# Kernel tuning notes

Hardware: AMD Instinct MI355X
Metric: run time of the kernel (lower is better)

Reference implementation:

```python
import jax, jax.numpy as jnp
import numpy as np

N_NODES = 50000
N_EDGES = 800000
IN_C, HID_C, OUT_C = 128, 256, 64


def _linear_params(key, fan_in, fan_out):
    kw, kb = jax.random.split(key)
    bound = 1.0 / np.sqrt(fan_in)
    w = jax.random.uniform(kw, (fan_in, fan_out), jnp.float32, -bound, bound)
    b = jax.random.uniform(kb, (fan_out,), jnp.float32, -bound, bound)
    return w, b


def setup_inputs() -> dict:
    key = jax.random.key(0)
    ks = jax.random.split(key, 8)
    x = jax.random.normal(ks[0], (N_NODES, IN_C), jnp.float32)
    edge_index = jax.random.randint(ks[1], (2, N_EDGES), 0, N_NODES, dtype=jnp.int64)
    w1a, b1a = _linear_params(ks[2], IN_C, HID_C)
    w1b, b1b = _linear_params(ks[3], HID_C, HID_C)
    w2a, b2a = _linear_params(ks[4], HID_C, HID_C)
    w2b, b2b = _linear_params(ks[5], HID_C, HID_C)
    w3a, b3a = _linear_params(ks[6], HID_C, HID_C)
    w3b, b3b = _linear_params(ks[7], HID_C, OUT_C)
    return {
        "x": x, "edge_index": edge_index,
        "w1a": w1a, "b1a": b1a, "w1b": w1b, "b1b": b1b,
        "w2a": w2a, "b2a": b2a, "w2b": w2b, "b2b": b2b,
        "w3a": w3a, "b3a": b3a, "w3b": w3b, "b3b": b3b,
    }


def _gin_conv(x, src, dst, wa, ba, wb, bb):
    # GINConv (eps=0): MLP( x + sum_{j->i} x_j )
    agg = jax.ops.segment_sum(x[src], dst, num_segments=N_NODES)  # [N, d]
    h = x + agg
    h = jnp.maximum(h @ wa + ba, 0.0)
    return h @ wb + bb


def reference(x, edge_index, w1a, b1a, w1b, b1b, w2a, b2a, w2b, b2b,
              w3a, b3a, w3b, b3b):
    src, dst = edge_index[0], edge_index[1]
    h = jnp.maximum(_gin_conv(x, src, dst, w1a, b1a, w1b, b1b), 0.0)
    h = jnp.maximum(_gin_conv(h, src, dst, w2a, b2a, w2b, b2b), 0.0)
    # output head: Linear -> ReLU -> Dropout(eval: identity) -> Linear
    h = jnp.maximum(h @ w3a + b3a, 0.0)
    return h @ w3b + b3b  # [N, OUT_C]
```

## Files before the change

### kernel.cpp

```cpp
#include <hip/hip_runtime.h>
#include <stdint.h>

#define N_NODES 50000
#define N_EDGES 800000
#define M_PAD   50048
#define NREP    4
#define MCAP    8
#define SCAP    24
#define BCAP    (MCAP + SCAP)
#define CSTR    50048
#define NPX     6256

typedef __attribute__((ext_vector_type(8))) short bf16x8;
typedef __attribute__((ext_vector_type(4))) float f32x4;
typedef __attribute__((ext_vector_type(4))) unsigned int u32x4;

__device__ __forceinline__ unsigned short f2b(float f){
    unsigned int u = __builtin_bit_cast(unsigned int, f);
    u += 0x7fffu + ((u >> 16) & 1u);
    return (unsigned short)(u >> 16);
}
__device__ __forceinline__ float b2f(unsigned short s){
    unsigned int u = ((unsigned int)s) << 16;
    return __builtin_bit_cast(float, u);
}
__device__ __forceinline__ float bcf(unsigned int u){
    return __builtin_bit_cast(float, u);
}

__device__ __forceinline__ void gl_lds16(const void* g, void* l){
    __builtin_amdgcn_global_load_lds(
        (const __attribute__((address_space(1))) void*)g,
        (__attribute__((address_space(3))) void*)l, 16, 0, 0);
}

__device__ __forceinline__ int t_off(int row, int us){
    return row * 256 + (((us >> 3) ^ (row & 7)) << 3) + (us & 7);
}

__device__ __forceinline__ void stage_w(const char* __restrict__ Wb, int kt, int K,
                                        int bytes, int tid, char* dst){
    for (int o = tid * 16; o < bytes; o += 8192){
        const int row = o >> 6, gs = ((o & 63) >> 4) ^ (row & 3);
        gl_lds16(Wb + ((size_t)row * K + kt * 32) * 2 + gs * 16, dst + o);
    }
}

__device__ __forceinline__ int pdeg(const int* __restrict__ cnt, int n){
    int v = 0;
#pragma unroll
    for (int r = 0; r < 4; ++r){
        int c = cnt[r * CSTR + n];
        v += (c > BCAP) ? BCAP : c;
    }
    return (v + 3) & ~3;
}

__global__ void k_x2b(const float* __restrict__ x, unsigned short* __restrict__ xs,
                      int* __restrict__ cnt){
    int gi = blockIdx.x * 256 + threadIdx.x;
    if (gi < NREP * CSTR) cnt[gi] = 0;
    size_t e0 = (size_t)gi * 8;
    if (e0 >= (size_t)M_PAD * 128) return;
    int node = (int)(e0 >> 7);
    int ch0  = (int)(e0 & 127);
    int sl = ch0 >> 5, wth = ch0 & 31;
    bf16x8 o;
    if (node < N_NODES){
        const float4* xp = (const float4*)(x + e0);
        float4 a = xp[0], b = xp[1];
        o[0] = (short)f2b(a.x); o[1] = (short)f2b(a.y);
        o[2] = (short)f2b(a.z); o[3] = (short)f2b(a.w);
        o[4] = (short)f2b(b.x); o[5] = (short)f2b(b.y);
        o[6] = (short)f2b(b.z); o[7] = (short)f2b(b.w);
    } else {
#pragma unroll
        for (int i = 0; i < 8; ++i) o[i] = 0;
    }
    *(bf16x8*)&xs[((size_t)(sl * 50048 + node)) * 32 + wth] = o;
}

__global__ __launch_bounds__(256) void k_scatter(const int* __restrict__ ei,
        int* __restrict__ cnt, unsigned short* __restrict__ mn,
        unsigned short* __restrict__ sp){
    const int x = blockIdx.x & 7;
    const int c = blockIdx.x >> 3;
    const int nlo = x * NPX, nhi = nlo + NPX;
    const int r = threadIdx.x & 3;
#pragma unroll
    for (int i = 0; i < 4; ++i){
        int e = c * 1024 + i * 256 + threadIdx.x;
        if (e < N_EDGES){
            int d = ei[N_EDGES + e];
            if (d >= nlo && d < nhi && (unsigned)d < N_NODES){
                unsigned s = (unsigned)ei[e];
                if (s < N_NODES){
                    int p = atomicAdd(&cnt[r * CSTR + d], 1);
                    int b = (d << 2) + r;
                    if (p < MCAP) mn[(b << 3) + p] = (unsigned short)s;
                    else if (p < BCAP) sp[b * SCAP + (p - MCAP)] = (unsigned short)s;
                }
            }
        }
    }
}

__global__ void k_scan1(const int* __restrict__ cnt, int* __restrict__ bsum){
    __shared__ int s[256];
    int t = threadIdx.x, n = blockIdx.x * 256 + t;
    int v = (n < M_PAD) ? pdeg(cnt, n) : 0;
    s[t] = v;
    __syncthreads();
    for (int off = 128; off > 0; off >>= 1){
        if (t < off) s[t] += s[t + off];
        __syncthreads();
    }
    if (t == 0) bsum[blockIdx.x] = s[0];
}

__global__ void k_scan2(const int* __restrict__ bsum, int* __restrict__ boff){
    __shared__ int s[256];
    int t = threadIdx.x;
    int v = (t < 196) ? bsum[t] : 0;
    s[t] = v;
    __syncthreads();
    for (int off = 1; off < 256; off <<= 1){
        int a = (t >= off) ? s[t - off] : 0;
        __syncthreads();
        s[t] += a;
        __syncthreads();
    }
    boff[t] = s[t] - v;
}

__global__ void k_scan3(const int* __restrict__ cnt, const int* __restrict__ boff,
                        int* __restrict__ mgoff){
    __shared__ int s[256];
    int t = threadIdx.x, n = blockIdx.x * 256 + t;
    int v = (n < M_PAD) ? pdeg(cnt, n) : 0;
    s[t] = v;
    __syncthreads();
    for (int off = 1; off < 256; off <<= 1){
        int a = (t >= off) ? s[t - off] : 0;
        __syncthreads();
        s[t] += a;
        __syncthreads();
    }
    if (n < M_PAD) mgoff[n] = boff[blockIdx.x] + s[t] - v;
}

__global__ void k_merge(const int* __restrict__ cnt, const int* __restrict__ mgoff,
                        const unsigned short* __restrict__ mn, const unsigned short* __restrict__ sp,
                        unsigned short* __restrict__ mg, int* __restrict__ mginfo,
                        unsigned short* __restrict__ lperm){
    __shared__ unsigned int keys[64];
    const int t = threadIdx.x;
    const int r = t & 3;
    const int n = blockIdx.x * 64 + (t >> 2);
    int c = cnt[r * CSTR + n];
    if (c > BCAP) c = BCAP;

    const unsigned short* src  = &mn[((n << 2) + r) << 3];
    const unsigned short* ssrc = &sp[((n << 2) + r) * SCAP];
    unsigned short v[BCAP];
    {
        ushort4 m0 = *(const ushort4*)(src);
        ushort4 m1 = *(const ushort4*)(src + 4);
        v[0]=m0.x; v[1]=m0.y; v[2]=m0.z; v[3]=m0.w;
        v[4]=m1.x; v[5]=m1.y; v[6]=m1.z; v[7]=m1.w;
#pragma unroll
        for (int q = 0; q < 6; ++q){
            ushort4 sq = *(const ushort4*)(ssrc + q * 4);
            v[8 + q*4 + 0] = sq.x; v[8 + q*4 + 1] = sq.y;
            v[8 + q*4 + 2] = sq.z; v[8 + q*4 + 3] = sq.w;
        }
    }
#pragma unroll
    for (int i = 0; i < BCAP; ++i)
        if (i >= c) v[i] = 0xFFFFu;

#pragma unroll
    for (int k = 2; k <= 32; k <<= 1){
#pragma unroll
        for (int j = k >> 1; j > 0; j >>= 1){
#pragma unroll
            for (int i = 0; i < 32; ++i){
                const int l = i ^ j;
                if (l > i){
                    const bool up = ((i & k) == 0);
                    unsigned short a = v[i], b = v[l];
                    bool sw = up ? (a > b) : (a < b);
                    unsigned short lo = sw ? b : a, hi = sw ? a : b;
                    v[i] = lo; v[l] = hi;
                }
            }
        }
    }

    int incl = c;
    int t1 = __shfl_up(incl, 1, 4); if (r >= 1) incl += t1;
    int t2 = __shfl_up(incl, 2, 4); if (r >= 2) incl += t2;
    const int excl = incl - c;
    const int total = __shfl(incl, 3, 4);
    const unsigned mb = (unsigned)mgoff[n];
#pragma unroll
    for (int i = 0; i < BCAP; ++i)
        if (i < c) mg[mb + excl + i] = v[i];
    if (r == 3){
        int grp = (total + 3) >> 2;
        mginfo[n] = ((int)mb << 6) | grp;
        for (int pos = total; pos < grp * 4; ++pos) mg[mb + pos] = (unsigned short)N_NODES;
        keys[t >> 2] = ((unsigned)grp << 6) | (unsigned)(t >> 2);
    }
    __syncthreads();
    for (int k = 2; k <= 64; k <<= 1){
        for (int j = k >> 1; j > 0; j >>= 1){
            if (t < 64){
                int l = t ^ j;
                if (l > t){
                    bool up = ((t & k) == 0);
                    unsigned a = keys[t], b = keys[l];
                    if (up ? (a > b) : (a < b)){ keys[t] = b; keys[l] = a; }
                }
            }
            __syncthreads();
        }
    }
    if (t < 64)
        lperm[blockIdx.x * 64 + t] = (unsigned short)(blockIdx.x * 64 + (keys[t] & 63));
}

template<int C, bool SPLIT>
__global__ __launch_bounds__(256) void k_aggx(const unsigned short* __restrict__ in,
        const int* __restrict__ mginfo, const unsigned short* __restrict__ mg,
        const unsigned short* __restrict__ lperm, unsigned short* __restrict__ out){
    constexpr int RS = C / 8;
    const int bid = blockIdx.x, w8 = bid & 7;
    int g, nbase;
    if (SPLIT){ g = w8 & 3; nbase = ((bid >> 3) + (w8 >> 2) * 391) * 64; }
    else      { g = w8;     nbase = (bid >> 3) * 64; }
    const int lane = threadIdx.x & 63, wid = threadIdx.x >> 6;
    const int qd = lane >> 2, lq = lane & 3;
    const int n = (int)lperm[nbase + wid * 16 + qd];
    const u32x4* __restrict__ xr = (const u32x4*)in;
    const unsigned sbu = (unsigned)g * 50048u;

    float alo[4], ahi[4];
    {
        u32x4 s = xr[(sbu + (unsigned)n) * 4u + (unsigned)lq];
#pragma unroll
        for (int j = 0; j < 4; ++j){
            alo[j] = bcf(s[j] << 16);
            ahi[j] = bcf(s[j] & 0xFFFF0000u);
        }
    }
    const int info = mginfo[n];
    const int grp = info & 63;
    const unsigned mbase = (unsigned)(info >> 6);
    for (int k = 0; k < grp; ++k){
        ushort4 jj = *(const ushort4*)&mg[mbase + (unsigned)(k * 4)];
        u32x4 v0 = xr[(sbu + jj.x) * 4u + lq];
        u32x4 v1 = xr[(sbu + jj.y) * 4u + lq];
        u32x4 v2 = xr[(sbu + jj.z) * 4u + lq];
        u32x4 v3 = xr[(sbu + jj.w) * 4u + lq];
#pragma unroll
        for (int j = 0; j < 4; ++j){
            alo[j] += (bcf(v0[j] << 16) + bcf(v1[j] << 16))
                    + (bcf(v2[j] << 16) + bcf(v3[j] << 16));
            ahi[j] += (bcf(v0[j] & 0xFFFF0000u) + bcf(v1[j] & 0xFFFF0000u))
                    + (bcf(v2[j] & 0xFFFF0000u) + bcf(v3[j] & 0xFFFF0000u));
        }
    }
    bf16x8 o;
#pragma unroll
    for (int j = 0; j < 4; ++j){
        o[2*j]     = (short)f2b(alo[j]);
        o[2*j + 1] = (short)f2b(ahi[j]);
    }
    *(bf16x8*)&out[((unsigned)n * RS + (unsigned)(g * 4 + lq)) * 8u] = o;
}

__global__ void k_wt_all(const float* w0, const float* w1, const float* w2,
                         const float* w3, const float* w4, const float* w5,
                         unsigned short* o0, unsigned short* o1, unsigned short* o2,
                         unsigned short* o3, unsigned short* o4, unsigned short* o5){
    const int Ks[6]  = {128, 256, 256, 256, 256, 256};
    const int Ns[6]  = {256, 256, 256, 256, 256,  64};
    const int NPs[6] = {256, 256, 256, 256, 256, 128};
    int s = blockIdx.y;
    const float* w = (s == 0) ? w0 : (s == 1) ? w1 : (s == 2) ? w2
                   : (s == 3) ? w3 : (s == 4) ? w4 : w5;
    unsigned short* o = (s == 0) ? o0 : (s == 1) ? o1 : (s == 2) ? o2
                      : (s == 3) ? o3 : (s == 4) ? o4 : o5;
    int K = Ks[s], N = Ns[s], NP = NPs[s];
    int idx = blockIdx.x * 256 + threadIdx.x;
    if (idx >= NP * K) return;
    int np = idx / K, k = idx - np * K;
    float v = (np < N) ? w[(size_t)k * N + np] : 0.f;
    o[idx] = f2b(v);
}

template<int K1, int NMID, int NOUT, bool RELU_OUT, bool SLICED>
__global__ __launch_bounds__(512) void k_mlp2(const unsigned short* __restrict__ A,
        const unsigned short* __restrict__ WA, const float* __restrict__ bA,
        const unsigned short* __restrict__ WB, const float* __restrict__ bB,
        void* __restrict__ out, int mstore){
    constexpr int NFA = NMID / 64;
    constexpr int NFB = NOUT / 64;
    constexpr int KTA = K1 / 32;
    constexpr int KTB = NMID / 32;
    __shared__ alignas(16) unsigned short As[2][128 * 32];
    __shared__ alignas(16) unsigned short Bs[2][256 * 32];
    __shared__ alignas(16) unsigned short T[128 * 256];
    const int tid  = threadIdx.x;
    const int lane = tid & 63;
    const int wave = tid >> 6;
    const int wm = wave >> 2, wn = wave & 3;
    const int c = lane & 15, qq = lane >> 4;
    const int sc = (qq ^ (c & 3)) * 8;
    const int row0 = blockIdx.x * 128;

    const f32x4 fzero = {0.f, 0.f, 0.f, 0.f};
    const char* Ab = (const char*)A;
    int cur = 0;

    {
        const int o = tid * 16;
        const int row = o >> 6, gs = ((o & 63) >> 4) ^ (row & 3);
        gl_lds16(Ab + ((size_t)(row0 + row) * K1) * 2 + gs * 16, (char*)As[0] + o);
    }
    stage_w((const char*)WA, 0, K1, NMID * 64, tid, (char*)Bs[0]);
    __syncthreads();

    {
        f32x4 acc[NFA][4];
#pragma unroll
        for (int nf = 0; nf < NFA; ++nf)
#pragma unroll
            for (int mf = 0; mf < 4; ++mf) acc[nf][mf] = fzero;
        for (int kt = 0; kt < KTA; ++kt){
            if (kt < KTA - 1){
                const int o = tid * 16;
                const int row = o >> 6, gs = ((o & 63) >> 4) ^ (row & 3);
                gl_lds16(Ab + ((size_t)(row0 + row) * K1 + (kt + 1) * 32) * 2 + gs * 16,
                         (char*)As[cur ^ 1] + o);
                stage_w((const char*)WA, kt + 1, K1, NMID * 64, tid, (char*)Bs[cur ^ 1]);
            } else {
                stage_w((const char*)WB, 0, NMID, NOUT * 64, tid, (char*)Bs[cur ^ 1]);
            }
            const unsigned short* AsC = As[cur];
            const unsigned short* BsC = Bs[cur];
            bf16x8 xf[4];
#pragma unroll
            for (int mf = 0; mf < 4; ++mf)
                xf[mf] = *(const bf16x8*)&AsC[(wm * 64 + mf * 16 + c) * 32 + sc];
#pragma unroll
            for (int nf = 0; nf < NFA; ++nf){
                bf16x8 wf = *(const bf16x8*)&BsC[((wn * NFA + nf) * 16 + c) * 32 + sc];
#pragma unroll
                for (int mf = 0; mf < 4; ++mf)
                    acc[nf][mf] = __builtin_amdgcn_mfma_f32_16x16x32_bf16(wf, xf[mf], acc[nf][mf], 0, 0, 0);
            }
            __syncthreads();
            cur ^= 1;
        }
#pragma unroll
        for (int nf = 0; nf < NFA; ++nf){
            const int nb = wn * (NFA * 16) + nf * 16 + qq * 4;
            const float4 bb = *(const float4*)&bA[nb];
#pragma unroll
            for (int mf = 0; mf < 4; ++mf){
                const int ml = wm * 64 + mf * 16 + c;
                float v0 = fmaxf(acc[nf][mf][0] + bb.x, 0.f);
                float v1 = fmaxf(acc[nf][mf][1] + bb.y, 0.f);
                float v2 = fmaxf(acc[nf][mf][2] + bb.z, 0.f);
                float v3 = fmaxf(acc[nf][mf][3] + bb.w, 0.f);
                uint2 p;
                p.x = (unsigned)f2b(v0) | ((unsigned)f2b(v1) << 16);
                p.y = (unsigned)f2b(v2) | ((unsigned)f2b(v3) << 16);
                *(uint2*)&T[t_off(ml, nb)] = p;
            }
        }
    }
    __syncthreads();

    {
        f32x4 acc[NFB][4];
#pragma unroll
        for (int nf = 0; nf < NFB; ++nf)
#pragma unroll
            for (int mf = 0; mf < 4; ++mf) acc[nf][mf] = fzero;
        for (int kt = 0; kt < KTB; ++kt){
            if (kt < KTB - 1)
                stage_w((const char*)WB, kt + 1, NMID, NOUT * 64, tid, (char*)Bs[cur ^ 1]);
            const unsigned short* BsC = Bs[cur];
            bf16x8 xf[4];
#pragma unroll
            for (int mf = 0; mf < 4; ++mf){
                const int rr = wm * 64 + mf * 16 + c;
                xf[mf] = *(const bf16x8*)&T[t_off(rr, kt * 32 + qq * 8)];
            }
#pragma unroll
            for (int nf = 0; nf < NFB; ++nf){
                bf16x8 wf = *(const bf16x8*)&BsC[((wn * NFB + nf) * 16 + c) * 32 + sc];
#pragma unroll
                for (int mf = 0; mf < 4; ++mf)
                    acc[nf][mf] = __builtin_amdgcn_mfma_f32_16x16x32_bf16(wf, xf[mf], acc[nf][mf], 0, 0, 0);
            }
            __syncthreads();
            cur ^= 1;
        }
#pragma unroll
        for (int nf = 0; nf < NFB; ++nf){
            const int nb = wn * (NFB * 16) + nf * 16 + qq * 4;
            const float4 bb = *(const float4*)&bB[nb];
#pragma unroll
            for (int mf = 0; mf < 4; ++mf){
                const int m = row0 + wm * 64 + mf * 16 + c;
                if (m < mstore){
                    float v0 = acc[nf][mf][0] + bb.x;
                    float v1 = acc[nf][mf][1] + bb.y;
                    float v2 = acc[nf][mf][2] + bb.z;
                    float v3 = acc[nf][mf][3] + bb.w;
                    if (RELU_OUT){
                        v0 = fmaxf(v0, 0.f); v1 = fmaxf(v1, 0.f);
                        v2 = fmaxf(v2, 0.f); v3 = fmaxf(v3, 0.f);
                    }
                    uint2 p;
                    p.x = (unsigned)f2b(v0) | ((unsigned)f2b(v1) << 16);
                    p.y = (unsigned)f2b(v2) | ((unsigned)f2b(v3) << 16);
                    if (SLICED){
                        if (m >= N_NODES){ p.x = 0; p.y = 0; }
                        *(uint2*)&((unsigned short*)out)[
                            ((size_t)((nb >> 5) * 50048 + m)) * 32 + (nb & 31)] = p;
                    } else {
                        *(uint2*)&((unsigned short*)out)[(size_t)m * NOUT + nb] = p;
                    }
                }
            }
        }
    }
}

__global__ __launch_bounds__(512) void k_mlp4(const unsigned short* __restrict__ A,
        const unsigned short* __restrict__ W1, const float* __restrict__ B1,
        const unsigned short* __restrict__ W2, const float* __restrict__ B2,
        const unsigned short* __restrict__ W3, const float* __restrict__ B3,
        const unsigned short* __restrict__ W4, const float* __restrict__ B4,
        float* __restrict__ out){
    __shared__ alignas(16) unsigned short As[2][128 * 32];
    __shared__ alignas(16) unsigned short Bs[2][256 * 32];
    __shared__ alignas(16) unsigned short T[128 * 256];
    const int tid  = threadIdx.x;
    const int lane = tid & 63;
    const int wave = tid >> 6;
    const int wm = wave >> 2, wn = wave & 3;
    const int c = lane & 15, qq = lane >> 4;
    const int sc = (qq ^ (c & 3)) * 8;
    const int row0 = blockIdx.x * 128;
    const f32x4 fzero = {0.f, 0.f, 0.f, 0.f};
    const char* Ab = (const char*)A;
    int cur = 0;

    {
        const int o = tid * 16;
        const int row = o >> 6, gs = ((o & 63) >> 4) ^ (row & 3);
        gl_lds16(Ab + ((size_t)(row0 + row) * 256) * 2 + gs * 16, (char*)As[0] + o);
    }
    stage_w((const char*)W1, 0, 256, 16384, tid, (char*)Bs[0]);
    __syncthreads();

    {
        f32x4 acc[4][4];
#pragma unroll
        for (int nf = 0; nf < 4; ++nf)
#pragma unroll
            for (int mf = 0; mf < 4; ++mf) acc[nf][mf] = fzero;
        for (int kt = 0; kt < 8; ++kt){
            if (kt < 7){
                const int o = tid * 16;
                const int row = o >> 6, gs = ((o & 63) >> 4) ^ (row & 3);
                gl_lds16(Ab + ((size_t)(row0 + row) * 256 + (kt + 1) * 32) * 2 + gs * 16,
                         (char*)As[cur ^ 1] + o);
                stage_w((const char*)W1, kt + 1, 256, 16384, tid, (char*)Bs[cur ^ 1]);
            } else {
                stage_w((const char*)W2, 0, 256, 16384, tid, (char*)Bs[cur ^ 1]);
            }
            const unsigned short* AsC = As[cur];
            const unsigned short* BsC = Bs[cur];
            bf16x8 xf[4];
#pragma unroll
            for (int mf = 0; mf < 4; ++mf)
                xf[mf] = *(const bf16x8*)&AsC[(wm * 64 + mf * 16 + c) * 32 + sc];
#pragma unroll
            for (int nf = 0; nf < 4; ++nf){
                bf16x8 wf = *(const bf16x8*)&BsC[((wn * 4 + nf) * 16 + c) * 32 + sc];
#pragma unroll
                for (int mf = 0; mf < 4; ++mf)
                    acc[nf][mf] = __builtin_amdgcn_mfma_f32_16x16x32_bf16(wf, xf[mf], acc[nf][mf], 0, 0, 0);
            }
            __syncthreads();
            cur ^= 1;
        }
#pragma unroll
        for (int nf = 0; nf < 4; ++nf){
            const int nb = wn * 64 + nf * 16 + qq * 4;
            const float4 bb = *(const float4*)&B1[nb];
#pragma unroll
            for (int mf = 0; mf < 4; ++mf){
                const int ml = wm * 64 + mf * 16 + c;
                float v0 = fmaxf(acc[nf][mf][0] + bb.x, 0.f);
                float v1 = fmaxf(acc[nf][mf][1] + bb.y, 0.f);
                float v2 = fmaxf(acc[nf][mf][2] + bb.z, 0.f);
                float v3 = fmaxf(acc[nf][mf][3] + bb.w, 0.f);
                uint2 p;
                p.x = (unsigned)f2b(v0) | ((unsigned)f2b(v1) << 16);
                p.y = (unsigned)f2b(v2) | ((unsigned)f2b(v3) << 16);
                *(uint2*)&T[t_off(ml, nb)] = p;
            }
        }
    }
    __syncthreads();

#pragma unroll 1
    for (int st = 0; st < 2; ++st){
        const char* Wb    = (const char*)(st == 0 ? W2 : W3);
        const char* Wnext = (const char*)(st == 0 ? W3 : W4);
        const int bytesNext = (st == 0) ? 16384 : 4096;
        const float* Bb = (st == 0 ? B2 : B3);
        f32x4 acc[4][4];
#pragma unroll
        for (int nf = 0; nf < 4; ++nf)
#pragma unroll
            for (int mf = 0; mf < 4; ++mf) acc[nf][mf] = fzero;
        for (int kt = 0; kt < 8; ++kt){
            if (kt < 7) stage_w(Wb, kt + 1, 256, 16384, tid, (char*)Bs[cur ^ 1]);
            else        stage_w(Wnext, 0, 256, bytesNext, tid, (char*)Bs[cur ^ 1]);
            const unsigned short* BsC = Bs[cur];
            bf16x8 xf[4];
#pragma unroll
            for (int mf = 0; mf < 4; ++mf){
                const int rr = wm * 64 + mf * 16 + c;
                xf[mf] = *(const bf16x8*)&T[t_off(rr, kt * 32 + qq * 8)];
            }
#pragma unroll
            for (int nf = 0; nf < 4; ++nf){
                bf16x8 wf = *(const bf16x8*)&BsC[((wn * 4 + nf) * 16 + c) * 32 + sc];
#pragma unroll
                for (int mf = 0; mf < 4; ++mf)
                    acc[nf][mf] = __builtin_amdgcn_mfma_f32_16x16x32_bf16(wf, xf[mf], acc[nf][mf], 0, 0, 0);
            }
            __syncthreads();
            cur ^= 1;
        }
#pragma unroll
        for (int nf = 0; nf < 4; ++nf){
            const int nb = wn * 64 + nf * 16 + qq * 4;
            const float4 bb = *(const float4*)&Bb[nb];
#pragma unroll
            for (int mf = 0; mf < 4; ++mf){
                const int ml = wm * 64 + mf * 16 + c;
                float v0 = fmaxf(acc[nf][mf][0] + bb.x, 0.f);
                float v1 = fmaxf(acc[nf][mf][1] + bb.y, 0.f);
                float v2 = fmaxf(acc[nf][mf][2] + bb.z, 0.f);
                float v3 = fmaxf(acc[nf][mf][3] + bb.w, 0.f);
                uint2 p;
                p.x = (unsigned)f2b(v0) | ((unsigned)f2b(v1) << 16);
                p.y = (unsigned)f2b(v2) | ((unsigned)f2b(v3) << 16);
                *(uint2*)&T[t_off(ml, nb)] = p;
            }
        }
        __syncthreads();
    }

    {
        f32x4 acc[4];
#pragma unroll
        for (int mf = 0; mf < 4; ++mf) acc[mf] = fzero;
        for (int kt = 0; kt < 8; ++kt){
            if (kt < 7) stage_w((const char*)W4, kt + 1, 256, 4096, tid, (char*)Bs[cur ^ 1]);
            const unsigned short* BsC = Bs[cur];
            bf16x8 xf[4];
#pragma unroll
            for (int mf = 0; mf < 4; ++mf){
                const int rr = wm * 64 + mf * 16 + c;
                xf[mf] = *(const bf16x8*)&T[t_off(rr, kt * 32 + qq * 8)];
            }
            bf16x8 wf = *(const bf16x8*)&BsC[(wn * 16 + c) * 32 + sc];
#pragma unroll
            for (int mf = 0; mf < 4; ++mf)
                acc[mf] = __builtin_amdgcn_mfma_f32_16x16x32_bf16(wf, xf[mf], acc[mf], 0, 0, 0);
            __syncthreads();
            cur ^= 1;
        }
        const int nb = wn * 16 + qq * 4;
        const float4 bb = *(const float4*)&B4[nb];
#pragma unroll
        for (int mf = 0; mf < 4; ++mf){
            const int m = row0 + wm * 64 + mf * 16 + c;
            if (m < N_NODES){
                float4 p = make_float4(acc[mf][0] + bb.x, acc[mf][1] + bb.y,
                                       acc[mf][2] + bb.z, acc[mf][3] + bb.w);
                *(float4*)&out[(size_t)m * 64 + nb] = p;
            }
        }
    }
}

extern "C" void kernel_launch(void* const* d_in, const int* in_sizes, int n_in,
                              void* d_out, int out_size, void* d_ws, size_t ws_size,
                              hipStream_t stream){
    const float* x   = (const float*)d_in[0];
    const int*   ei  = (const int*)d_in[1];
    const float* w1a = (const float*)d_in[2];
    const float* b1a = (const float*)d_in[3];
    const float* w1b = (const float*)d_in[4];
    const float* b1b = (const float*)d_in[5];
    const float* w2a = (const float*)d_in[6];
    const float* b2a = (const float*)d_in[7];
    const float* w2b = (const float*)d_in[8];
    const float* b2b = (const float*)d_in[9];
    const float* w3a = (const float*)d_in[10];
    const float* b3a = (const float*)d_in[11];
    const float* w3b = (const float*)d_in[12];
    const float* b3b = (const float*)d_in[13];

    char* ws = (char*)d_ws;
    size_t off = 0;
    auto take = [&](size_t bytes) -> char* {
        off = (off + 255) & ~(size_t)255;
        char* p = ws + off;
        off += bytes;
        return p;
    };
    unsigned short* xs1  = (unsigned short*)take((size_t)4 * 50048 * 32 * 2);
    unsigned short* g1   = (unsigned short*)take((size_t)M_PAD * 128 * 2);
    unsigned short* h1s  = (unsigned short*)take((size_t)8 * 50048 * 32 * 2);
    unsigned short* g2   = (unsigned short*)take((size_t)M_PAD * 256 * 2);
    unsigned short* wt1a = (unsigned short*)take(256 * 128 * 2);
    unsigned short* wt1b = (unsigned short*)take(256 * 256 * 2);
    unsigned short* wt2a = (unsigned short*)take(256 * 256 * 2);
    unsigned short* wt2b = (unsigned short*)take(256 * 256 * 2);
    unsigned short* wt3a = (unsigned short*)take(256 * 256 * 2);
    unsigned short* wt3b = (unsigned short*)take(128 * 256 * 2);
    int*            cnt  = (int*)take((size_t)NREP * CSTR * 4);
    unsigned short* mn   = (unsigned short*)take((size_t)M_PAD * 4 * MCAP * 2);
    unsigned short* sp   = (unsigned short*)take((size_t)M_PAD * 4 * SCAP * 2);
    unsigned short* mg   = (unsigned short*)take((size_t)1100000 * 2);
    int*            mgoff  = (int*)take((size_t)M_PAD * 4);
    int*            mginfo = (int*)take((size_t)M_PAD * 4);
    int*            bsum = (int*)take(256 * 4);
    int*            boff = (int*)take(256 * 4);
    unsigned short* lperm = (unsigned short*)take((size_t)M_PAD * 2);

    k_x2b<<<(M_PAD * 128 / 8 + 255) / 256, 256, 0, stream>>>(x, xs1, cnt);
    k_scatter<<<782 * 8, 256, 0, stream>>>(ei, cnt, mn, sp);
    k_scan1<<<196, 256, 0, stream>>>(cnt, bsum);
    k_scan2<<<1,   256, 0, stream>>>(bsum, boff);
    k_scan3<<<196, 256, 0, stream>>>(cnt, boff, mgoff);
    k_merge<<<782, 256, 0, stream>>>(cnt, mgoff, mn, sp, mg, mginfo, lperm);
    k_wt_all<<<dim3(256, 6), 256, 0, stream>>>(w1a, w1b, w2a, w2b, w3a, w3b,
                                               wt1a, wt1b, wt2a, wt2b, wt3a, wt3b);

    k_aggx<128, true ><<<391 * 8, 256, 0, stream>>>(xs1, mginfo, mg, lperm, g1);
    k_mlp2<128, 256, 256, true, true><<<391, 512, 0, stream>>>(
        g1, wt1a, b1a, wt1b, b1b, h1s, M_PAD);
    k_aggx<256, false><<<782 * 8, 256, 0, stream>>>(h1s, mginfo, mg, lperm, g2);
    k_mlp4<<<391, 512, 0, stream>>>(
        g2, wt2a, b2a, wt2b, b2b, wt3a, b3a, wt3b, b3b, (float*)d_out);
}
```

Measured before the change: 212.2 us.

## Load MLP operands directly from global memory instead of LDS staging

Removes the double-buffered LDS staging of activation and weight tiles in the fused MLP kernels. Each wave now reads its A and W fragments straight from global memory into registers, with the k-loop fully unrolled. This drops the per-k-tile __syncthreads and cuts LDS use from about 112KB to 64KB per block, which may allow more blocks per CU. In exchange, every wave issues redundant global loads of the weights and activations, relying on the L1/L2 caches, and the loads are no longer overlapped with compute through prefetching.

```diff
diff --git a/kernel.cpp b/kernel.cpp
--- a/kernel.cpp
+++ b/kernel.cpp
@@ -36,14 +36,6 @@
 
 __device__ __forceinline__ int t_off(int row, int us){
     return row * 256 + (((us >> 3) ^ (row & 7)) << 3) + (us & 7);
-}
-
-__device__ __forceinline__ void stage_w(const char* __restrict__ Wb, int kt, int K,
-                                        int bytes, int tid, char* dst){
-    for (int o = tid * 16; o < bytes; o += 8192){
-        const int row = o >> 6, gs = ((o & 63) >> 4) ^ (row & 3);
-        gl_lds16(Wb + ((size_t)row * K + kt * 32) * 2 + gs * 16, dst + o);
-    }
 }
 
 __device__ __forceinline__ int pdeg(const int* __restrict__ cnt, int n){
@@ -309,28 +301,14 @@
     constexpr int NFB = NOUT / 64;
     constexpr int KTA = K1 / 32;
     constexpr int KTB = NMID / 32;
-    __shared__ alignas(16) unsigned short As[2][128 * 32];
-    __shared__ alignas(16) unsigned short Bs[2][256 * 32];
     __shared__ alignas(16) unsigned short T[128 * 256];
     const int tid  = threadIdx.x;
     const int lane = tid & 63;
     const int wave = tid >> 6;
     const int wm = wave >> 2, wn = wave & 3;
     const int c = lane & 15, qq = lane >> 4;
-    const int sc = (qq ^ (c & 3)) * 8;
     const int row0 = blockIdx.x * 128;
-
     const f32x4 fzero = {0.f, 0.f, 0.f, 0.f};
-    const char* Ab = (const char*)A;
-    int cur = 0;
-
-    {
-        const int o = tid * 16;
-        const int row = o >> 6, gs = ((o & 63) >> 4) ^ (row & 3);
-        gl_lds16(Ab + ((size_t)(row0 + row) * K1) * 2 + gs * 16, (char*)As[0] + o);
-    }
-    stage_w((const char*)WA, 0, K1, NMID * 64, tid, (char*)Bs[0]);
-    __syncthreads();
 
     {
         f32x4 acc[NFA][4];
@@ -338,31 +316,27 @@
         for (int nf = 0; nf < NFA; ++nf)
 #pragma unroll
             for (int mf = 0; mf < 4; ++mf) acc[nf][mf] = fzero;
+        const unsigned short* Ab[4];
+#pragma unroll
+        for (int mf = 0; mf < 4; ++mf)
+            Ab[mf] = A + (size_t)(row0 + wm * 64 + mf * 16 + c) * K1 + qq * 8;
+        const unsigned short* Wb[NFA];
+#pragma unroll
+        for (int nf = 0; nf < NFA; ++nf)
+            Wb[nf] = WA + (size_t)((wn * NFA + nf) * 16 + c) * K1 + qq * 8;
+#pragma unroll
         for (int kt = 0; kt < KTA; ++kt){
-            if (kt < KTA - 1){
-                const int o = tid * 16;
-                const int row = o >> 6, gs = ((o & 63) >> 4) ^ (row & 3);
-                gl_lds16(Ab + ((size_t)(row0 + row) * K1 + (kt + 1) * 32) * 2 + gs * 16,
-                         (char*)As[cur ^ 1] + o);
-                stage_w((const char*)WA, kt + 1, K1, NMID * 64, tid, (char*)Bs[cur ^ 1]);
-            } else {
-                stage_w((const char*)WB, 0, NMID, NOUT * 64, tid, (char*)Bs[cur ^ 1]);
-            }
-            const unsigned short* AsC = As[cur];
-            const unsigned short* BsC = Bs[cur];
             bf16x8 xf[4];
 #pragma unroll
             for (int mf = 0; mf < 4; ++mf)
-                xf[mf] = *(const bf16x8*)&AsC[(wm * 64 + mf * 16 + c) * 32 + sc];
+                xf[mf] = *(const bf16x8*)(Ab[mf] + kt * 32);
 #pragma unroll
             for (int nf = 0; nf < NFA; ++nf){
-                bf16x8 wf = *(const bf16x8*)&BsC[((wn * NFA + nf) * 16 + c) * 32 + sc];
+                bf16x8 wf = *(const bf16x8*)(Wb[nf] + kt * 32);
 #pragma unroll
                 for (int mf = 0; mf < 4; ++mf)
                     acc[nf][mf] = __builtin_amdgcn_mfma_f32_16x16x32_bf16(wf, xf[mf], acc[nf][mf], 0, 0, 0);
             }
-            __syncthreads();
-            cur ^= 1;
         }
 #pragma unroll
         for (int nf = 0; nf < NFA; ++nf){
@@ -390,10 +364,12 @@
         for (int nf = 0; nf < NFB; ++nf)
 #pragma unroll
             for (int mf = 0; mf < 4; ++mf) acc[nf][mf] = fzero;
+        const unsigned short* Wb[NFB];
+#pragma unroll
+        for (int nf = 0; nf < NFB; ++nf)
+            Wb[nf] = WB + (size_t)((wn * NFB + nf) * 16 + c) * NMID + qq * 8;
+#pragma unroll
         for (int kt = 0; kt < KTB; ++kt){
-            if (kt < KTB - 1)
-                stage_w((const char*)WB, kt + 1, NMID, NOUT * 64, tid, (char*)Bs[cur ^ 1]);
-            const unsigned short* BsC = Bs[cur];
             bf16x8 xf[4];
 #pragma unroll
             for (int mf = 0; mf < 4; ++mf){
@@ -402,13 +378,11 @@
             }
 #pragma unroll
             for (int nf = 0; nf < NFB; ++nf){
-                bf16x8 wf = *(const bf16x8*)&BsC[((wn * NFB + nf) * 16 + c) * 32 + sc];
+                bf16x8 wf = *(const bf16x8*)(Wb[nf] + kt * 32);
 #pragma unroll
                 for (int mf = 0; mf < 4; ++mf)
                     acc[nf][mf] = __builtin_amdgcn_mfma_f32_16x16x32_bf16(wf, xf[mf], acc[nf][mf], 0, 0, 0);
             }
-            __syncthreads();
-            cur ^= 1;
         }
 #pragma unroll
         for (int nf = 0; nf < NFB; ++nf){
@@ -448,27 +422,14 @@
         const unsigned short* __restrict__ W3, const float* __restrict__ B3,
         const unsigned short* __restrict__ W4, const float* __restrict__ B4,
         float* __restrict__ out){
-    __shared__ alignas(16) unsigned short As[2][128 * 32];
-    __shared__ alignas(16) unsigned short Bs[2][256 * 32];
     __shared__ alignas(16) unsigned short T[128 * 256];
     const int tid  = threadIdx.x;
     const int lane = tid & 63;
     const int wave = tid >> 6;
     const int wm = wave >> 2, wn = wave & 3;
     const int c = lane & 15, qq = lane >> 4;
-    const int sc = (qq ^ (c & 3)) * 8;
     const int row0 = blockIdx.x * 128;
     const f32x4 fzero = {0.f, 0.f, 0.f, 0.f};
-    const char* Ab = (const char*)A;
-    int cur = 0;
-
-    {
-        const int o = tid * 16;
-        const int row = o >> 6, gs = ((o & 63) >> 4) ^ (row & 3);
-        gl_lds16(Ab + ((size_t)(row0 + row) * 256) * 2 + gs * 16, (char*)As[0] + o);
-    }
-    stage_w((const char*)W1, 0, 256, 16384, tid, (char*)Bs[0]);
-    __syncthreads();
 
     {
         f32x4 acc[4][4];
@@ -476,31 +437,27 @@
         for (int nf = 0; nf < 4; ++nf)
 #pragma unroll
             for (int mf = 0; mf < 4; ++mf) acc[nf][mf] = fzero;
+        const unsigned short* Ab[4];
+#pragma unroll
+        for (int mf = 0; mf < 4; ++mf)
+            Ab[mf] = A + (size_t)(row0 + wm * 64 + mf * 16 + c) * 256 + qq * 8;
+        const unsigned short* Wb[4];
+#pragma unroll
+        for (int nf = 0; nf < 4; ++nf)
+            Wb[nf] = W1 + (size_t)((wn * 4 + nf) * 16 + c) * 256 + qq * 8;
+#pragma unroll
         for (int kt = 0; kt < 8; ++kt){
-            if (kt < 7){
-                const int o = tid * 16;
-                const int row = o >> 6, gs = ((o & 63) >> 4) ^ (row & 3);
-                gl_lds16(Ab + ((size_t)(row0 + row) * 256 + (kt + 1) * 32) * 2 + gs * 16,
-                         (char*)As[cur ^ 1] + o);
-                stage_w((const char*)W1, kt + 1, 256, 16384, tid, (char*)Bs[cur ^ 1]);
-            } else {
-                stage_w((const char*)W2, 0, 256, 16384, tid, (char*)Bs[cur ^ 1]);
-            }
-            const unsigned short* AsC = As[cur];
-            const unsigned short* BsC = Bs[cur];
             bf16x8 xf[4];
 #pragma unroll
             for (int mf = 0; mf < 4; ++mf)
-                xf[mf] = *(const bf16x8*)&AsC[(wm * 64 + mf * 16 + c) * 32 + sc];
+                xf[mf] = *(const bf16x8*)(Ab[mf] + kt * 32);
 #pragma unroll
             for (int nf = 0; nf < 4; ++nf){
-                bf16x8 wf = *(const bf16x8*)&BsC[((wn * 4 + nf) * 16 + c) * 32 + sc];
+                bf16x8 wf = *(const bf16x8*)(Wb[nf] + kt * 32);
 #pragma unroll
                 for (int mf = 0; mf < 4; ++mf)
                     acc[nf][mf] = __builtin_amdgcn_mfma_f32_16x16x32_bf16(wf, xf[mf], acc[nf][mf], 0, 0, 0);
             }
-            __syncthreads();
-            cur ^= 1;
         }
 #pragma unroll
         for (int nf = 0; nf < 4; ++nf){
@@ -524,19 +481,19 @@
 
 #pragma unroll 1
     for (int st = 0; st < 2; ++st){
-        const char* Wb    = (const char*)(st == 0 ? W2 : W3);
-        const char* Wnext = (const char*)(st == 0 ? W3 : W4);
-        const int bytesNext = (st == 0) ? 16384 : 4096;
+        const unsigned short* Wt = (st == 0 ? W2 : W3);
         const float* Bb = (st == 0 ? B2 : B3);
         f32x4 acc[4][4];
 #pragma unroll
         for (int nf = 0; nf < 4; ++nf)
 #pragma unroll
             for (int mf = 0; mf < 4; ++mf) acc[nf][mf] = fzero;
+        const unsigned short* Wb[4];
+#pragma unroll
+        for (int nf = 0; nf < 4; ++nf)
+            Wb[nf] = Wt + (size_t)((wn * 4 + nf) * 16 + c) * 256 + qq * 8;
+#pragma unroll
         for (int kt = 0; kt < 8; ++kt){
-            if (kt < 7) stage_w(Wb, kt + 1, 256, 16384, tid, (char*)Bs[cur ^ 1]);
-            else        stage_w(Wnext, 0, 256, bytesNext, tid, (char*)Bs[cur ^ 1]);
-            const unsigned short* BsC = Bs[cur];
             bf16x8 xf[4];
 #pragma unroll
             for (int mf = 0; mf < 4; ++mf){
@@ -545,14 +502,13 @@
             }
 #pragma unroll
             for (int nf = 0; nf < 4; ++nf){
-                bf16x8 wf = *(const bf16x8*)&BsC[((wn * 4 + nf) * 16 + c) * 32 + sc];
+                bf16x8 wf = *(const bf16x8*)(Wb[nf] + kt * 32);
 #pragma unroll
                 for (int mf = 0; mf < 4; ++mf)
                     acc[nf][mf] = __builtin_amdgcn_mfma_f32_16x16x32_bf16(wf, xf[mf], acc[nf][mf], 0, 0, 0);
             }
-            __syncthreads();
-            cur ^= 1;
-        }
+        }
+        __syncthreads();
 #pragma unroll
         for (int nf = 0; nf < 4; ++nf){
             const int nb = wn * 64 + nf * 16 + qq * 4;
@@ -577,21 +533,19 @@
         f32x4 acc[4];
 #pragma unroll
         for (int mf = 0; mf < 4; ++mf) acc[mf] = fzero;
+        const unsigned short* Wb = W4 + (size_t)(wn * 16 + c) * 256 + qq * 8;
+#pragma unroll
         for (int kt = 0; kt < 8; ++kt){
-            if (kt < 7) stage_w((const char*)W4, kt + 1, 256, 4096, tid, (char*)Bs[cur ^ 1]);
-            const unsigned short* BsC = Bs[cur];
             bf16x8 xf[4];
 #pragma unroll
             for (int mf = 0; mf < 4; ++mf){
                 const int rr = wm * 64 + mf * 16 + c;
                 xf[mf] = *(const bf16x8*)&T[t_off(rr, kt * 32 + qq * 8)];
             }
-            bf16x8 wf = *(const bf16x8*)&BsC[(wn * 16 + c) * 32 + sc];
+            bf16x8 wf = *(const bf16x8*)(Wb + kt * 32);
 #pragma unroll
             for (int mf = 0; mf < 4; ++mf)
                 acc[mf] = __builtin_amdgcn_mfma_f32_16x16x32_bf16(wf, xf[mf], acc[mf], 0, 0, 0);
-            __syncthreads();
-            cur ^= 1;
         }
         const int nb = wn * 16 + qq * 4;
         const float4 bb = *(const float4*)&B4[nb];
```

Measured after the change: 253.8 us. 1.2x slower.
